# Optimization experiments

Measured on AMD Instinct MI355X. Metric: run time of the kernel, lower is better.

Reference implementation:

```python
import jax, jax.numpy as jnp
import numpy as np

N_NODES = 150000       # original nodes
N_FRAG_NODES = 300000  # nodes duplicated across fragments
N_FRAGS = 30000        # number of fragments (segments of fragments_batch)
E = 1200000            # edges in combined fragment graph
D = 128                # nhid


def seg_mean(x, seg, num):
    s = jax.ops.segment_sum(x, seg, num_segments=num)
    c = jax.ops.segment_sum(jnp.ones((x.shape[0], 1), x.dtype), seg, num_segments=num)
    return s / jnp.maximum(c, 1.0)


def setup_inputs() -> dict:
    key = jax.random.key(0)
    ks = jax.random.split(key, 8)
    x = jax.random.normal(ks[0], (N_NODES, D), dtype=jnp.float32)
    mapper = jax.random.randint(ks[1], (N_FRAG_NODES,), 0, N_NODES)
    batch = jnp.sort(jax.random.randint(ks[2], (N_FRAG_NODES,), 0, N_FRAGS))
    edge_index = jax.random.randint(ks[3], (2, E), 0, N_FRAG_NODES)
    W_u = jax.random.normal(ks[4], (D, D), dtype=jnp.float32) * 0.05
    b_u = jnp.zeros((D,), dtype=jnp.float32)
    W_gcn = jax.random.normal(ks[5], (D, D), dtype=jnp.float32) * 0.05
    b_gcn = jnp.zeros((D,), dtype=jnp.float32)
    return {
        "x": x,
        "fragments_nodes_mapper": mapper,
        "fragments_batch": batch,
        "edge_index": edge_index,
        "W_u": W_u,
        "b_u": b_u,
        "W_gcn": W_gcn,
        "b_gcn": b_gcn,
        "i": 0,
    }


def gcn_conv(x, edge_index, W, b, n):
    # PyG GCNConv: add self loops, symmetric normalization D^-1/2 (A+I) D^-1/2, then linear.
    xw = x @ W  # [n, D]
    loops = jnp.arange(n, dtype=edge_index.dtype)
    row = jnp.concatenate([edge_index[0], loops])  # source
    col = jnp.concatenate([edge_index[1], loops])  # target (aggregation index)
    deg = jax.ops.segment_sum(jnp.ones(row.shape[0], x.dtype), col, num_segments=n)
    dinv = jnp.where(deg > 0, jax.lax.rsqrt(jnp.maximum(deg, 1.0)), 0.0)
    norm = dinv[row] * dinv[col]  # [E+n]
    msg = xw[row] * norm[:, None]
    out = jax.ops.segment_sum(msg, col, num_segments=n)
    return out + b


def reference(x, fragments_nodes_mapper, fragments_batch, edge_index, W_u, b_u, W_gcn, b_gcn, i):
    if i == 0:
        x = x[fragments_nodes_mapper]  # gather: [N_FRAG_NODES, D]
    # fragment-level mean pooling, broadcast back to fragment-nodes
    fragment = seg_mean(x, fragments_batch, N_FRAGS)[fragments_batch]
    # U[i-1]: MLP(nhid, nhid, nlayer=1, with_final_activation=True) -> Linear + ReLU
    x = x + jax.nn.relu(fragment @ W_u + b_u)
    # pool duplicated fragment-nodes back onto original nodes, then re-broadcast
    x = seg_mean(x, fragments_nodes_mapper, N_NODES)[fragments_nodes_mapper]
    # GCN over the combined fragment graph
    x = gcn_conv(x, edge_index, W_gcn, b_gcn, N_FRAG_NODES)
    fragment_x = seg_mean(x, fragments_batch, N_FRAGS)  # [N_FRAGS, D]
    return (fragment_x, x)
```

## Files before the change

kernel.cpp:

```cpp
#include <hip/hip_runtime.h>
#include <hip/hip_bf16.h>

#define N_NODES      150000
#define N_FRAG_NODES 300000
#define N_FRAGS      30000
#define NEDGE        1200000
#define NCNT         (N_NODES + N_FRAG_NODES)
#define D            128
#define DV           32
#define SCAN_TILE    1024

typedef __attribute__((ext_vector_type(8))) short short8;
typedef __attribute__((ext_vector_type(8))) unsigned short u16x8;
typedef __attribute__((ext_vector_type(4))) float f32x4;
typedef __attribute__((ext_vector_type(2))) int i32x2;

__device__ __forceinline__ unsigned short f2bf(float f) {
    unsigned u = __float_as_uint(f);
    u = (u + 0x7FFFu + ((u >> 16) & 1u)) >> 16;
    return (unsigned short)u;
}
__device__ __forceinline__ float bf2f(unsigned short u) {
    return __uint_as_float((unsigned)u << 16);
}

__global__ void k_prep(const int* __restrict__ mapper, const int* __restrict__ batch,
                       const int* __restrict__ ecol, int* __restrict__ mcnt,
                       int* __restrict__ ccnt, int* __restrict__ startb) {
    int i = blockIdx.x * blockDim.x + threadIdx.x;
    if (i < NEDGE) atomicAdd(&ccnt[ecol[i]], 1);
    if (i < N_FRAG_NODES) atomicAdd(&mcnt[mapper[i]], 1);
    if (i <= N_FRAGS) {
        int lo = 0, hi = N_FRAG_NODES;
        while (lo < hi) { int mid = (lo + hi) >> 1; if (batch[mid] < i) lo = mid + 1; else hi = mid; }
        startb[i] = lo;
    }
}

__global__ void k_scan_tile(const int* __restrict__ cnt, int* __restrict__ combst,
                            int* __restrict__ tsum) {
    __shared__ int buf[SCAN_TILE];
    int tid = threadIdx.x;
    int i = blockIdx.x * SCAN_TILE + tid;
    int v = (i < NCNT) ? cnt[i] : 0;
    buf[tid] = v;
    __syncthreads();
    for (int off = 1; off < SCAN_TILE; off <<= 1) {
        int t = (tid >= off) ? buf[tid - off] : 0;
        __syncthreads();
        buf[tid] += t;
        __syncthreads();
    }
    if (i < NCNT) combst[i] = buf[tid] - v;
    if (tid == SCAN_TILE - 1) tsum[blockIdx.x] = buf[tid];
}

__global__ void k_scan_tsum(int* __restrict__ tsum, int ntiles,
                            int* __restrict__ mstart, int* __restrict__ cstart) {
    __shared__ int buf[SCAN_TILE];
    int tid = threadIdx.x;
    int v = (tid < ntiles) ? tsum[tid] : 0;
    buf[tid] = v;
    __syncthreads();
    for (int off = 1; off < SCAN_TILE; off <<= 1) {
        int t = (tid >= off) ? buf[tid - off] : 0;
        __syncthreads();
        buf[tid] += t;
        __syncthreads();
    }
    if (tid < ntiles) tsum[tid] = buf[tid] - v;
    if (tid == SCAN_TILE - 1) {
        mstart[N_NODES] = N_FRAG_NODES;
        cstart[N_FRAG_NODES] = buf[tid] - N_FRAG_NODES;
    }
}

__global__ void k_scan_add(const int* __restrict__ combst, const int* __restrict__ tsum,
                           int* __restrict__ mstart, int* __restrict__ cstart) {
    int i = blockIdx.x * blockDim.x + threadIdx.x;
    if (i >= NCNT) return;
    int v = combst[i] + tsum[i >> 10];
    if (i < N_NODES) mstart[i] = v;
    else cstart[i - N_NODES] = v - N_FRAG_NODES;
}

__global__ void k_frag_mean(const float4* __restrict__ x4, const int* __restrict__ mapper,
                            const int* __restrict__ startb, ushort4* __restrict__ frag16) {
    int g = threadIdx.x >> 5, lane = threadIdx.x & 31;
    int b = blockIdx.x * 8 + g;
    if (b >= N_FRAGS) return;
    int s = startb[b], e = startb[b + 1];
    float4 sA = {0.f, 0.f, 0.f, 0.f}, sB = {0.f, 0.f, 0.f, 0.f};
    int j = s;
    for (; j + 2 <= e; j += 2) {
        int m0 = mapper[j], m1 = mapper[j + 1];
        float4 v0 = x4[(size_t)m0 * DV + lane];
        float4 v1 = x4[(size_t)m1 * DV + lane];
        sA.x += v0.x; sA.y += v0.y; sA.z += v0.z; sA.w += v0.w;
        sB.x += v1.x; sB.y += v1.y; sB.z += v1.z; sB.w += v1.w;
    }
    if (j < e) {
        int m0 = mapper[j];
        float4 v0 = x4[(size_t)m0 * DV + lane];
        sA.x += v0.x; sA.y += v0.y; sA.z += v0.z; sA.w += v0.w;
    }
    float c = (float)(e - s); if (c < 1.f) c = 1.f;
    float inv = 1.f / c;
    ushort4 r = {f2bf((sA.x + sB.x) * inv), f2bf((sA.y + sB.y) * inv),
                 f2bf((sA.z + sB.z) * inv), f2bf((sA.w + sB.w) * inv)};
    frag16[(size_t)b * DV + lane] = r;
}

__global__ void k_build_wfrag(const float* __restrict__ W, short* __restrict__ wfrag) {
    int t = threadIdx.x;
    for (int e = t; e < 2048; e += 256) {
        int nt = e >> 8;
        int kk = (e >> 6) & 3;
        int lane = e & 63;
        int col = nt * 16 + (lane & 15);
        int kb = kk * 32 + ((lane >> 4) << 3);
        short8 v;
        #pragma unroll
        for (int j = 0; j < 8; ++j) v[j] = (short)f2bf(W[(kb + j) * D + col]);
        ((short8*)wfrag)[e] = v;
    }
}

template <bool RELU, bool BIAS>
__global__ void __launch_bounds__(256)
k_rowmat_mfma(const unsigned short* __restrict__ src16, const short* __restrict__ wfrag,
              const float* __restrict__ bias, unsigned short* __restrict__ dst16, int rows) {
    __shared__ short8 wl[2048];
    int tid = threadIdx.x;
    for (int e = tid; e < 2048; e += 256) wl[e] = ((const short8*)wfrag)[e];
    __syncthreads();
    int wv = tid >> 6, lane = tid & 63;
    int lrow = lane & 15;
    int lk8 = (lane >> 4);
    float bv[8];
    #pragma unroll
    for (int nt = 0; nt < 8; ++nt) bv[nt] = BIAS ? bias[nt * 16 + lrow] : 0.f;

    int chunk = blockIdx.x * 64;
    {
        int r = chunk + wv * 16 + lrow;
        short8 af[4];
        if (r < rows) {
            const short8* rowp = (const short8*)(src16 + (size_t)r * D);
            #pragma unroll
            for (int kk = 0; kk < 4; ++kk) af[kk] = rowp[kk * 4 + lk8];
        } else {
            #pragma unroll
            for (int kk = 0; kk < 4; ++kk) af[kk] = (short8)0;
        }
        f32x4 acc[8];
        #pragma unroll
        for (int nt = 0; nt < 8; ++nt) acc[nt] = (f32x4)0.f;
        #pragma unroll
        for (int nt = 0; nt < 8; ++nt) {
            #pragma unroll
            for (int kk = 0; kk < 4; ++kk)
                acc[nt] = __builtin_amdgcn_mfma_f32_16x16x32_bf16(
                              af[kk], wl[(nt * 4 + kk) * 64 + lane], acc[nt], 0, 0, 0);
        }
        int orow0 = chunk + wv * 16 + ((lane >> 4) << 2);
        #pragma unroll
        for (int nt = 0; nt < 8; ++nt) {
            int col = nt * 16 + lrow;
            #pragma unroll
            for (int reg = 0; reg < 4; ++reg) {
                int orow = orow0 + reg;
                if (orow < rows) {
                    float v = acc[nt][reg] + bv[nt];
                    if (RELU) v = fmaxf(v, 0.f);
                    dst16[(size_t)orow * D + col] = f2bf(v);
                }
            }
        }
    }
}

__global__ void k_sval(const int* __restrict__ mapper, const int* __restrict__ cstart,
                       int2* __restrict__ sval) {
    int r = blockIdx.x * blockDim.x + threadIdx.x;
    if (r >= N_FRAG_NODES) return;
    int2 v;
    v.x = mapper[r];
    v.y = __float_as_int(rsqrtf((float)(cstart[r + 1] - cstart[r] + 1)));
    sval[r] = v;
}

__global__ void k_fill(const int* __restrict__ mapper, const int* __restrict__ batch,
                       const int* __restrict__ erow, const int* __restrict__ ecol,
                       const int* __restrict__ mstart, int* __restrict__ mcnt,
                       int* __restrict__ mvals, const int* __restrict__ cstart,
                       int* __restrict__ ccnt, const int2* __restrict__ sval,
                       int2* __restrict__ erecs) {
    int i = blockIdx.x * blockDim.x + threadIdx.x;
    if (i < N_FRAG_NODES) {
        int k = mapper[i];
        int pos = atomicSub(&mcnt[k], 1) - 1;
        mvals[mstart[k] + pos] = batch[i];
    }
    if (i < NEDGE) {
        int c = ecol[i], r = erow[i];
        int pos = atomicSub(&ccnt[c], 1) - 1;
        erecs[cstart[c] + pos] = sval[r];
    }
}

__global__ void k_pool_csr(const float4* __restrict__ x4, const u16x8* __restrict__ fragu8,
                           const int* __restrict__ mstart, const int* __restrict__ mvals,
                           u16x8* __restrict__ pooled8) {
    int g = threadIdx.x >> 4, lane = threadIdx.x & 15;
    int n = blockIdx.x * 16 + g;
    if (n >= N_NODES) return;
    int s = mstart[n], e = mstart[n + 1];
    u16x8 out = (u16x8)0;
    if (e > s) {
        float accA[8], accB[8];
        #pragma unroll
        for (int j = 0; j < 8; ++j) { accA[j] = 0.f; accB[j] = 0.f; }
        int t = s;
        for (; t + 2 <= e; t += 2) {
            int b0 = mvals[t], b1 = mvals[t + 1];
            u16x8 u0 = fragu8[(size_t)b0 * 16 + lane];
            u16x8 u1 = fragu8[(size_t)b1 * 16 + lane];
            #pragma unroll
            for (int j = 0; j < 8; ++j) {
                accA[j] += bf2f(u0[j]);
                accB[j] += bf2f(u1[j]);
            }
        }
        if (t < e) {
            int b0 = mvals[t];
            u16x8 u0 = fragu8[(size_t)b0 * 16 + lane];
            #pragma unroll
            for (int j = 0; j < 8; ++j) accA[j] += bf2f(u0[j]);
        }
        float inv = 1.f / (float)(e - s);
        float4 xv0 = x4[(size_t)n * DV + lane * 2];
        float4 xv1 = x4[(size_t)n * DV + lane * 2 + 1];
        out[0] = f2bf(fmaf(accA[0] + accB[0], inv, xv0.x));
        out[1] = f2bf(fmaf(accA[1] + accB[1], inv, xv0.y));
        out[2] = f2bf(fmaf(accA[2] + accB[2], inv, xv0.z));
        out[3] = f2bf(fmaf(accA[3] + accB[3], inv, xv0.w));
        out[4] = f2bf(fmaf(accA[4] + accB[4], inv, xv1.x));
        out[5] = f2bf(fmaf(accA[5] + accB[5], inv, xv1.y));
        out[6] = f2bf(fmaf(accA[6] + accB[6], inv, xv1.z));
        out[7] = f2bf(fmaf(accA[7] + accB[7], inv, xv1.w));
    }
    pooled8[(size_t)n * 16 + lane] = out;
}

__global__ void k_gcn_gather(const int* __restrict__ cstart, const int2* __restrict__ sval,
                             const i32x2* __restrict__ erecs, const u16x8* __restrict__ pw8,
                             const float* __restrict__ bgcn, f32x4* __restrict__ xout4) {
    int g = threadIdx.x >> 4, lane = threadIdx.x & 15;
    int c = blockIdx.x * 16 + g;
    if (c >= N_FRAG_NODES) return;
    int s = cstart[c], e = cstart[c + 1];
    int2 sv = sval[c];
    float dc = __int_as_float(sv.y);
    float acc0[8], acc1[8], acc2[8], acc3[8];
    #pragma unroll
    for (int j = 0; j < 8; ++j) { acc0[j] = 0.f; acc1[j] = 0.f; acc2[j] = 0.f; acc3[j] = 0.f; }
    int t = s;
    for (; t + 4 <= e; t += 4) {
        i32x2 r0 = __builtin_nontemporal_load(&erecs[t]);
        i32x2 r1 = __builtin_nontemporal_load(&erecs[t + 1]);
        i32x2 r2 = __builtin_nontemporal_load(&erecs[t + 2]);
        i32x2 r3 = __builtin_nontemporal_load(&erecs[t + 3]);
        u16x8 u0 = pw8[(size_t)r0.x * 16 + lane];
        u16x8 u1 = pw8[(size_t)r1.x * 16 + lane];
        u16x8 u2 = pw8[(size_t)r2.x * 16 + lane];
        u16x8 u3 = pw8[(size_t)r3.x * 16 + lane];
        float w0 = __int_as_float(r0.y), w1 = __int_as_float(r1.y);
        float w2 = __int_as_float(r2.y), w3 = __int_as_float(r3.y);
        #pragma unroll
        for (int j = 0; j < 8; ++j) {
            acc0[j] = fmaf(bf2f(u0[j]), w0, acc0[j]);
            acc1[j] = fmaf(bf2f(u1[j]), w1, acc1[j]);
            acc2[j] = fmaf(bf2f(u2[j]), w2, acc2[j]);
            acc3[j] = fmaf(bf2f(u3[j]), w3, acc3[j]);
        }
    }
    for (; t < e; ++t) {
        i32x2 r0 = __builtin_nontemporal_load(&erecs[t]);
        u16x8 u0 = pw8[(size_t)r0.x * 16 + lane];
        float w0 = __int_as_float(r0.y);
        #pragma unroll
        for (int j = 0; j < 8; ++j) acc0[j] = fmaf(bf2f(u0[j]), w0, acc0[j]);
    }
    u16x8 su = pw8[(size_t)sv.x * 16 + lane];
    float dc2 = dc * dc;
    const float4* bg4 = (const float4*)bgcn;
    float4 b0 = bg4[lane * 2], b1 = bg4[lane * 2 + 1];
    float o[8];
    #pragma unroll
    for (int j = 0; j < 8; ++j)
        o[j] = fmaf((acc0[j] + acc1[j]) + (acc2[j] + acc3[j]), dc, bf2f(su[j]) * dc2);
    f32x4 o0 = {o[0] + b0.x, o[1] + b0.y, o[2] + b0.z, o[3] + b0.w};
    f32x4 o1 = {o[4] + b1.x, o[5] + b1.y, o[6] + b1.z, o[7] + b1.w};
    __builtin_nontemporal_store(o0, &xout4[(size_t)c * DV + lane * 2]);
    __builtin_nontemporal_store(o1, &xout4[(size_t)c * DV + lane * 2 + 1]);
}

__global__ void k_frag_x(const float4* __restrict__ x4, const int* __restrict__ startb,
                         float4* __restrict__ fout4) {
    int g = threadIdx.x >> 5, lane = threadIdx.x & 31;
    int b = blockIdx.x * 8 + g;
    if (b >= N_FRAGS) return;
    int s = startb[b], e = startb[b + 1];
    float4 sA = {0.f, 0.f, 0.f, 0.f}, sB = {0.f, 0.f, 0.f, 0.f};
    int j = s;
    for (; j + 2 <= e; j += 2) {
        float4 v0 = x4[(size_t)j * DV + lane];
        float4 v1 = x4[(size_t)(j + 1) * DV + lane];
        sA.x += v0.x; sA.y += v0.y; sA.z += v0.z; sA.w += v0.w;
        sB.x += v1.x; sB.y += v1.y; sB.z += v1.z; sB.w += v1.w;
    }
    if (j < e) {
        float4 v0 = x4[(size_t)j * DV + lane];
        sA.x += v0.x; sA.y += v0.y; sA.z += v0.z; sA.w += v0.w;
    }
    float4 r = {0.f, 0.f, 0.f, 0.f};
    if (e > s) {
        float inv = 1.f / (float)(e - s);
        r.x = (sA.x + sB.x) * inv; r.y = (sA.y + sB.y) * inv;
        r.z = (sA.z + sB.z) * inv; r.w = (sA.w + sB.w) * inv;
    }
    fout4[(size_t)b * DV + lane] = r;
}

extern "C" void kernel_launch(void* const* d_in, const int* in_sizes, int n_in,
                              void* d_out, int out_size, void* d_ws, size_t ws_size,
                              hipStream_t stream) {
    const float* x      = (const float*)d_in[0];
    const int*   mapper = (const int*)d_in[1];
    const int*   batch  = (const int*)d_in[2];
    const int*   erow   = (const int*)d_in[3];
    const int*   ecol   = erow + NEDGE;
    const float* W_u    = (const float*)d_in[4];
    const float* b_u    = (const float*)d_in[5];
    const float* W_gcn  = (const float*)d_in[6];
    const float* b_gcn  = (const float*)d_in[7];

    float* fout = (float*)d_out;
    float* xout = fout + (size_t)N_FRAGS * D;

    short*  wfragU   = (short*)d_ws;
    short*  wfragG   = wfragU + 16384;
    int2*   erecs    = (int2*)(wfragG + 16384);
    int2*   sval     = erecs + NEDGE;
    unsigned short* frag16   = (unsigned short*)(sval + N_FRAG_NODES);
    unsigned short* pooled16 = frag16 + (size_t)N_FRAGS * D;
    int*    startb = (int*)(pooled16 + (size_t)N_NODES * D);
    int*    mstart = startb + (N_FRAGS + 1);
    int*    cstart = mstart + (N_NODES + 1);
    int*    mcnt   = cstart + (N_FRAG_NODES + 1);
    int*    ccnt   = mcnt + N_NODES;
    int*    mvals  = ccnt + N_FRAG_NODES;
    int*    combst = mvals + N_FRAG_NODES;
    int*    tsum   = combst + NCNT;

    hipMemsetAsync(mcnt, 0, (size_t)NCNT * sizeof(int), stream);

    k_build_wfrag<<<1, 256, 0, stream>>>(W_u, wfragU);
    k_build_wfrag<<<1, 256, 0, stream>>>(W_gcn, wfragG);

    k_prep<<<(NEDGE + 255) / 256, 256, 0, stream>>>(mapper, batch, ecol, mcnt, ccnt, startb);

    int ntiles = (NCNT + SCAN_TILE - 1) / SCAN_TILE;
    k_scan_tile<<<ntiles, SCAN_TILE, 0, stream>>>(mcnt, combst, tsum);
    k_scan_tsum<<<1, SCAN_TILE, 0, stream>>>(tsum, ntiles, mstart, cstart);
    k_scan_add<<<(NCNT + 255) / 256, 256, 0, stream>>>(combst, tsum, mstart, cstart);

    k_frag_mean<<<(N_FRAGS + 7) / 8, 256, 0, stream>>>((const float4*)x, mapper, startb,
                                                       (ushort4*)frag16);
    k_rowmat_mfma<true, true><<<(N_FRAGS + 63) / 64, 256, 0, stream>>>(
        frag16, wfragU, b_u, frag16, N_FRAGS);

    k_sval<<<(N_FRAG_NODES + 255) / 256, 256, 0, stream>>>(mapper, cstart, sval);
    k_fill<<<(NEDGE + 255) / 256, 256, 0, stream>>>(mapper, batch, erow, ecol,
                                                    mstart, mcnt, mvals,
                                                    cstart, ccnt, sval, erecs);

    k_pool_csr<<<(N_NODES + 15) / 16, 256, 0, stream>>>((const float4*)x, (const u16x8*)frag16,
                                                        mstart, mvals, (u16x8*)pooled16);
    k_rowmat_mfma<false, false><<<(N_NODES + 63) / 64, 256, 0, stream>>>(
        pooled16, wfragG, nullptr, pooled16, N_NODES);

    k_gcn_gather<<<(N_FRAG_NODES + 15) / 16, 256, 0, stream>>>(cstart, sval, (const i32x2*)erecs,
                                                               (const u16x8*)pooled16,
                                                               b_gcn, (f32x4*)xout);
    k_frag_x<<<(N_FRAGS + 7) / 8, 256, 0, stream>>>((const float4*)xout, startb, (float4*)fout);
}
```

Baseline: 373.5 us.

## Pre-convert x to bf16, fuse sval into scan, and widen frag-mean gathers

Converts x to a bf16 copy inside the prep kernel and switches frag-mean and pool_csr to gather 16-byte bf16 rows, with frag-mean processing 16 fragments per block and a 4-way unrolled accumulate. The separate k_sval kernel is folded into k_scan_add, which reads the edge counts directly from the count buffer. The erecs loads drop their nontemporal hint. The intent is to halve gather traffic on x and remove one launch, at the cost of an extra bf16 write pass over x and reduced precision in the x and fragment sums.

```diff
diff --git a/kernel.cpp b/kernel.cpp
--- a/kernel.cpp
+++ b/kernel.cpp
@@ -8,6 +8,7 @@
 #define NCNT         (N_NODES + N_FRAG_NODES)
 #define D            128
 #define DV           32
+#define NX16         (N_NODES * 16)
 #define SCAN_TILE    1024
 
 typedef __attribute__((ext_vector_type(8))) short short8;
@@ -25,8 +26,9 @@
 }
 
 __global__ void k_prep(const int* __restrict__ mapper, const int* __restrict__ batch,
-                       const int* __restrict__ ecol, int* __restrict__ mcnt,
-                       int* __restrict__ ccnt, int* __restrict__ startb) {
+                       const int* __restrict__ ecol, const float4* __restrict__ x4,
+                       int* __restrict__ mcnt, int* __restrict__ ccnt,
+                       int* __restrict__ startb, u16x8* __restrict__ x16) {
     int i = blockIdx.x * blockDim.x + threadIdx.x;
     if (i < NEDGE) atomicAdd(&ccnt[ecol[i]], 1);
     if (i < N_FRAG_NODES) atomicAdd(&mcnt[mapper[i]], 1);
@@ -34,6 +36,18 @@
         int lo = 0, hi = N_FRAG_NODES;
         while (lo < hi) { int mid = (lo + hi) >> 1; if (batch[mid] < i) lo = mid + 1; else hi = mid; }
         startb[i] = lo;
+    }
+    #pragma unroll
+    for (int rep = 0; rep < 2; ++rep) {
+        int slot = i + rep * NEDGE;
+        if (slot < NX16) {
+            float4 v0 = x4[(size_t)slot * 2];
+            float4 v1 = x4[(size_t)slot * 2 + 1];
+            u16x8 o;
+            o[0] = f2bf(v0.x); o[1] = f2bf(v0.y); o[2] = f2bf(v0.z); o[3] = f2bf(v0.w);
+            o[4] = f2bf(v1.x); o[5] = f2bf(v1.y); o[6] = f2bf(v1.z); o[7] = f2bf(v1.w);
+            x16[slot] = o;
+        }
     }
 }
 
@@ -76,39 +90,59 @@
 }
 
 __global__ void k_scan_add(const int* __restrict__ combst, const int* __restrict__ tsum,
-                           int* __restrict__ mstart, int* __restrict__ cstart) {
+                           int* __restrict__ mstart, int* __restrict__ cstart,
+                           const int* __restrict__ mapper, const int* __restrict__ cnt,
+                           int2* __restrict__ sval) {
     int i = blockIdx.x * blockDim.x + threadIdx.x;
     if (i >= NCNT) return;
     int v = combst[i] + tsum[i >> 10];
-    if (i < N_NODES) mstart[i] = v;
-    else cstart[i - N_NODES] = v - N_FRAG_NODES;
-}
-
-__global__ void k_frag_mean(const float4* __restrict__ x4, const int* __restrict__ mapper,
-                            const int* __restrict__ startb, ushort4* __restrict__ frag16) {
-    int g = threadIdx.x >> 5, lane = threadIdx.x & 31;
-    int b = blockIdx.x * 8 + g;
+    if (i < N_NODES) {
+        mstart[i] = v;
+    } else {
+        int r = i - N_NODES;
+        cstart[r] = v - N_FRAG_NODES;
+        int2 s;
+        s.x = mapper[r];
+        s.y = __float_as_int(rsqrtf((float)(cnt[i] + 1)));
+        sval[r] = s;
+    }
+}
+
+__global__ void k_frag_mean(const u16x8* __restrict__ x16, const int* __restrict__ mapper,
+                            const int* __restrict__ startb, u16x8* __restrict__ frag16) {
+    int g = threadIdx.x >> 4, lane = threadIdx.x & 15;
+    int b = blockIdx.x * 16 + g;
     if (b >= N_FRAGS) return;
     int s = startb[b], e = startb[b + 1];
-    float4 sA = {0.f, 0.f, 0.f, 0.f}, sB = {0.f, 0.f, 0.f, 0.f};
+    float a0[8], a1[8], a2[8], a3[8];
+    #pragma unroll
+    for (int j = 0; j < 8; ++j) { a0[j] = 0.f; a1[j] = 0.f; a2[j] = 0.f; a3[j] = 0.f; }
     int j = s;
-    for (; j + 2 <= e; j += 2) {
-        int m0 = mapper[j], m1 = mapper[j + 1];
-        float4 v0 = x4[(size_t)m0 * DV + lane];
-        float4 v1 = x4[(size_t)m1 * DV + lane];
-        sA.x += v0.x; sA.y += v0.y; sA.z += v0.z; sA.w += v0.w;
-        sB.x += v1.x; sB.y += v1.y; sB.z += v1.z; sB.w += v1.w;
-    }
-    if (j < e) {
+    for (; j + 4 <= e; j += 4) {
+        int m0 = mapper[j], m1 = mapper[j + 1], m2 = mapper[j + 2], m3 = mapper[j + 3];
+        u16x8 v0 = x16[(size_t)m0 * 16 + lane];
+        u16x8 v1 = x16[(size_t)m1 * 16 + lane];
+        u16x8 v2 = x16[(size_t)m2 * 16 + lane];
+        u16x8 v3 = x16[(size_t)m3 * 16 + lane];
+        #pragma unroll
+        for (int k = 0; k < 8; ++k) {
+            a0[k] += bf2f(v0[k]); a1[k] += bf2f(v1[k]);
+            a2[k] += bf2f(v2[k]); a3[k] += bf2f(v3[k]);
+        }
+    }
+    for (; j < e; ++j) {
         int m0 = mapper[j];
-        float4 v0 = x4[(size_t)m0 * DV + lane];
-        sA.x += v0.x; sA.y += v0.y; sA.z += v0.z; sA.w += v0.w;
+        u16x8 v0 = x16[(size_t)m0 * 16 + lane];
+        #pragma unroll
+        for (int k = 0; k < 8; ++k) a0[k] += bf2f(v0[k]);
     }
     float c = (float)(e - s); if (c < 1.f) c = 1.f;
     float inv = 1.f / c;
-    ushort4 r = {f2bf((sA.x + sB.x) * inv), f2bf((sA.y + sB.y) * inv),
-                 f2bf((sA.z + sB.z) * inv), f2bf((sA.w + sB.w) * inv)};
-    frag16[(size_t)b * DV + lane] = r;
+    u16x8 r;
+    #pragma unroll
+    for (int k = 0; k < 8; ++k)
+        r[k] = f2bf(((a0[k] + a1[k]) + (a2[k] + a3[k])) * inv);
+    frag16[(size_t)b * 16 + lane] = r;
 }
 
 __global__ void k_build_wfrag(const float* __restrict__ W, short* __restrict__ wfrag) {
@@ -180,16 +214,6 @@
     }
 }
 
-__global__ void k_sval(const int* __restrict__ mapper, const int* __restrict__ cstart,
-                       int2* __restrict__ sval) {
-    int r = blockIdx.x * blockDim.x + threadIdx.x;
-    if (r >= N_FRAG_NODES) return;
-    int2 v;
-    v.x = mapper[r];
-    v.y = __float_as_int(rsqrtf((float)(cstart[r + 1] - cstart[r] + 1)));
-    sval[r] = v;
-}
-
 __global__ void k_fill(const int* __restrict__ mapper, const int* __restrict__ batch,
                        const int* __restrict__ erow, const int* __restrict__ ecol,
                        const int* __restrict__ mstart, int* __restrict__ mcnt,
@@ -209,7 +233,7 @@
     }
 }
 
-__global__ void k_pool_csr(const float4* __restrict__ x4, const u16x8* __restrict__ fragu8,
+__global__ void k_pool_csr(const u16x8* __restrict__ x16, const u16x8* __restrict__ fragu8,
                            const int* __restrict__ mstart, const int* __restrict__ mvals,
                            u16x8* __restrict__ pooled8) {
     int g = threadIdx.x >> 4, lane = threadIdx.x & 15;
@@ -239,22 +263,16 @@
             for (int j = 0; j < 8; ++j) accA[j] += bf2f(u0[j]);
         }
         float inv = 1.f / (float)(e - s);
-        float4 xv0 = x4[(size_t)n * DV + lane * 2];
-        float4 xv1 = x4[(size_t)n * DV + lane * 2 + 1];
-        out[0] = f2bf(fmaf(accA[0] + accB[0], inv, xv0.x));
-        out[1] = f2bf(fmaf(accA[1] + accB[1], inv, xv0.y));
-        out[2] = f2bf(fmaf(accA[2] + accB[2], inv, xv0.z));
-        out[3] = f2bf(fmaf(accA[3] + accB[3], inv, xv0.w));
-        out[4] = f2bf(fmaf(accA[4] + accB[4], inv, xv1.x));
-        out[5] = f2bf(fmaf(accA[5] + accB[5], inv, xv1.y));
-        out[6] = f2bf(fmaf(accA[6] + accB[6], inv, xv1.z));
-        out[7] = f2bf(fmaf(accA[7] + accB[7], inv, xv1.w));
+        u16x8 xv = x16[(size_t)n * 16 + lane];
+        #pragma unroll
+        for (int j = 0; j < 8; ++j)
+            out[j] = f2bf(fmaf(accA[j] + accB[j], inv, bf2f(xv[j])));
     }
     pooled8[(size_t)n * 16 + lane] = out;
 }
 
 __global__ void k_gcn_gather(const int* __restrict__ cstart, const int2* __restrict__ sval,
-                             const i32x2* __restrict__ erecs, const u16x8* __restrict__ pw8,
+                             const int2* __restrict__ erecs, const u16x8* __restrict__ pw8,
                              const float* __restrict__ bgcn, f32x4* __restrict__ xout4) {
     int g = threadIdx.x >> 4, lane = threadIdx.x & 15;
     int c = blockIdx.x * 16 + g;
@@ -267,10 +285,10 @@
     for (int j = 0; j < 8; ++j) { acc0[j] = 0.f; acc1[j] = 0.f; acc2[j] = 0.f; acc3[j] = 0.f; }
     int t = s;
     for (; t + 4 <= e; t += 4) {
-        i32x2 r0 = __builtin_nontemporal_load(&erecs[t]);
-        i32x2 r1 = __builtin_nontemporal_load(&erecs[t + 1]);
-        i32x2 r2 = __builtin_nontemporal_load(&erecs[t + 2]);
-        i32x2 r3 = __builtin_nontemporal_load(&erecs[t + 3]);
+        int2 r0 = erecs[t];
+        int2 r1 = erecs[t + 1];
+        int2 r2 = erecs[t + 2];
+        int2 r3 = erecs[t + 3];
         u16x8 u0 = pw8[(size_t)r0.x * 16 + lane];
         u16x8 u1 = pw8[(size_t)r1.x * 16 + lane];
         u16x8 u2 = pw8[(size_t)r2.x * 16 + lane];
@@ -286,7 +304,7 @@
         }
     }
     for (; t < e; ++t) {
-        i32x2 r0 = __builtin_nontemporal_load(&erecs[t]);
+        int2 r0 = erecs[t];
         u16x8 u0 = pw8[(size_t)r0.x * 16 + lane];
         float w0 = __int_as_float(r0.y);
         #pragma unroll
@@ -353,7 +371,8 @@
     short*  wfragG   = wfragU + 16384;
     int2*   erecs    = (int2*)(wfragG + 16384);
     int2*   sval     = erecs + NEDGE;
-    unsigned short* frag16   = (unsigned short*)(sval + N_FRAG_NODES);
+    unsigned short* x16      = (unsigned short*)(sval + N_FRAG_NODES);
+    unsigned short* frag16   = x16 + (size_t)N_NODES * D;
     unsigned short* pooled16 = frag16 + (size_t)N_FRAGS * D;
     int*    startb = (int*)(pooled16 + (size_t)N_NODES * D);
     int*    mstart = startb + (N_FRAGS + 1);
@@ -369,29 +388,30 @@
     k_build_wfrag<<<1, 256, 0, stream>>>(W_u, wfragU);
     k_build_wfrag<<<1, 256, 0, stream>>>(W_gcn, wfragG);
 
-    k_prep<<<(NEDGE + 255) / 256, 256, 0, stream>>>(mapper, batch, ecol, mcnt, ccnt, startb);
+    k_prep<<<(NEDGE + 255) / 256, 256, 0, stream>>>(mapper, batch, ecol, (const float4*)x,
+                                                    mcnt, ccnt, startb, (u16x8*)x16);
 
     int ntiles = (NCNT + SCAN_TILE - 1) / SCAN_TILE;
     k_scan_tile<<<ntiles, SCAN_TILE, 0, stream>>>(mcnt, combst, tsum);
     k_scan_tsum<<<1, SCAN_TILE, 0, stream>>>(tsum, ntiles, mstart, cstart);
-    k_scan_add<<<(NCNT + 255) / 256, 256, 0, stream>>>(combst, tsum, mstart, cstart);
-
-    k_frag_mean<<<(N_FRAGS + 7) / 8, 256, 0, stream>>>((const float4*)x, mapper, startb,
-                                                       (ushort4*)frag16);
+    k_scan_add<<<(NCNT + 255) / 256, 256, 0, stream>>>(combst, tsum, mstart, cstart,
+                                                       mapper, mcnt, sval);
+
+    k_frag_mean<<<(N_FRAGS + 15) / 16, 256, 0, stream>>>((const u16x8*)x16, mapper, startb,
+                                                         (u16x8*)frag16);
     k_rowmat_mfma<true, true><<<(N_FRAGS + 63) / 64, 256, 0, stream>>>(
         frag16, wfragU, b_u, frag16, N_FRAGS);
 
-    k_sval<<<(N_FRAG_NODES + 255) / 256, 256, 0, stream>>>(mapper, cstart, sval);
     k_fill<<<(NEDGE + 255) / 256, 256, 0, stream>>>(mapper, batch, erow, ecol,
                                                     mstart, mcnt, mvals,
                                                     cstart, ccnt, sval, erecs);
 
-    k_pool_csr<<<(N_NODES + 15) / 16, 256, 0, stream>>>((const float4*)x, (const u16x8*)frag16,
+    k_pool_csr<<<(N_NODES + 15) / 16, 256, 0, stream>>>((const u16x8*)x16, (const u16x8*)frag16,
                                                         mstart, mvals, (u16x8*)pooled16);
     k_rowmat_mfma<false, false><<<(N_NODES + 63) / 64, 256, 0, stream>>>(
         pooled16, wfragG, nullptr, pooled16, N_NODES);
 
-    k_gcn_gather<<<(N_FRAG_NODES + 15) / 16, 256, 0, stream>>>(cstart, sval, (const i32x2*)erecs,
+    k_gcn_gather<<<(N_FRAG_NODES + 15) / 16, 256, 0, stream>>>(cstart, sval, erecs,
                                                                (const u16x8*)pooled16,
                                                                b_gcn, (f32x4*)xout);
     k_frag_x<<<(N_FRAGS + 7) / 8, 256, 0, stream>>>((const float4*)xout, startb, (float4*)fout);
```

New measurement: 360.4 us. 3.5% less time.
